# Optimization experiments

Measured on AMD Instinct MI355X. Metric: run time of the kernel, lower is better.

Reference implementation:

```python
import jax, jax.numpy as jnp
import numpy as np

D_MODEL, N_HEADS = 768, 12
D_K = D_MODEL // N_HEADS
NEG = -1e9


def setup_inputs() -> dict:
    key = jax.random.key(0)
    ks = jax.random.split(key, 12)
    B, S, D = 2, 4096, D_MODEL
    s = 1.0 / np.sqrt(D)
    inp = {
        'query': jax.random.normal(ks[0], (B, S, D), jnp.float32),
        'key': jax.random.normal(ks[1], (B, S, D), jnp.float32),
        'value': jax.random.normal(ks[2], (B, S, D), jnp.float32),
        'mask': jnp.ones((B, S), jnp.int32),
        'Wq': jax.random.normal(ks[3], (D, D), jnp.float32) * s,
        'bq': jnp.zeros((D,), jnp.float32),
        'Wk': jax.random.normal(ks[4], (D, D), jnp.float32) * s,
        'bk': jnp.zeros((D,), jnp.float32),
        'Wv': jax.random.normal(ks[5], (D, D), jnp.float32) * s,
        'bv': jnp.zeros((D,), jnp.float32),
        'Wo': jax.random.normal(ks[6], (D, D), jnp.float32) * s,
        'bo': jnp.zeros((D,), jnp.float32),
    }
    return inp


def reference(query, key, value, mask, Wq, bq, Wk, bk, Wv, bv, Wo, bo):
    B, Sq, D = query.shape
    Sk = key.shape[1]
    # torch Linear: x @ W.T + b; weights stored [out, in]
    def proj(x, W, b, S):
        return (x @ W.T + b).reshape(B, S, N_HEADS, D_K).transpose(0, 2, 1, 3)
    Q = proj(query, Wq, bq, Sq)   # [B,H,Sq,Dk]
    K = proj(key, Wk, bk, Sk)
    V = proj(value, Wv, bv, Sk)
    scores = jnp.einsum('bhqd,bhkd->bhqk', Q, K) / jnp.sqrt(jnp.float32(D_K))
    # padding mask on keys: [B,1,1,Sk]
    scores = jnp.where(mask[:, None, None, :] == 0, NEG, scores)
    # causal mask (triu, diagonal=1)
    causal = jnp.triu(jnp.ones((Sq, Sk), bool), k=1)
    scores = jnp.where(causal[None, None], NEG, scores)
    attn = jax.nn.softmax(scores, axis=-1)
    out = jnp.einsum('bhqk,bhkd->bhqd', attn, V)
    out = out.transpose(0, 2, 1, 3).reshape(B, Sq, D)
    return out @ Wo.T + bo
```

## Files before the change

### kernel.cpp

```cpp
#include <hip/hip_runtime.h>
#include <hip/hip_bf16.h>

#define D_MODEL 768
#define N_HEADS 12
#define D_K     64
#define NEG_INF (-1e9f)
#define SCALE_Q 0.1803368801111154f
#define W_ELEMS (D_MODEL * D_MODEL)

typedef __attribute__((ext_vector_type(8))) short          bf16x8;
typedef __attribute__((ext_vector_type(4))) float          floatx4;
typedef __attribute__((ext_vector_type(4))) unsigned short ushortx4;
typedef __attribute__((ext_vector_type(2))) unsigned int   uintx2;
typedef __attribute__((ext_vector_type(4))) unsigned int   uintx4;

static __device__ __forceinline__ unsigned short f2bf(float f) {
    unsigned u = __builtin_bit_cast(unsigned, f);
    u += 0x7FFFu + ((u >> 16) & 1u);
    return (unsigned short)(u >> 16);
}

static __device__ __forceinline__ float exp2_hw(float x) {
#if __has_builtin(__builtin_amdgcn_exp2f)
    return __builtin_amdgcn_exp2f(x);
#else
    return __builtin_exp2f(x);
#endif
}

static __device__ __forceinline__ float rcp_hw(float x) {
#if __has_builtin(__builtin_amdgcn_rcpf)
    return __builtin_amdgcn_rcpf(x);
#else
    return 1.f / x;
#endif
}

static __device__ __forceinline__ void gload_lds16(const void* g, void* l) {
    __builtin_amdgcn_global_load_lds(
        (const __attribute__((address_space(1))) void*)g,
        (__attribute__((address_space(3))) void*)l, 16, 0, 0);
}

__global__ __launch_bounds__(256) void convert_w4(
    const float* __restrict__ W0, const float* __restrict__ W1,
    const float* __restrict__ W2, const float* __restrict__ W3,
    unsigned short* __restrict__ out)
{
    const float* src[4] = {W0, W1, W2, W3};
    const float* W = src[blockIdx.y];
    unsigned short* o = out + (size_t)blockIdx.y * W_ELEMS;
    const int i = (blockIdx.x * 256 + threadIdx.x) * 4;
    float4 v = *(const float4*)(W + i);
    ushortx4 h = { f2bf(v.x), f2bf(v.y), f2bf(v.z), f2bf(v.w) };
    *(ushortx4*)(o + i) = h;
}

__global__ __launch_bounds__(256) void convert_a3(
    const float* __restrict__ A0, const float* __restrict__ A1,
    const float* __restrict__ A2,
    unsigned short* __restrict__ O0, unsigned short* __restrict__ O1,
    unsigned short* __restrict__ O2)
{
    const int z = blockIdx.y;
    const float* A = (z == 0) ? A0 : (z == 1) ? A1 : A2;
    unsigned short* O = (z == 0) ? O0 : (z == 1) ? O1 : O2;
    const int i = (blockIdx.x * 256 + threadIdx.x) * 4;
    float4 v = *(const float4*)(A + i);
    ushortx4 h = { f2bf(v.x), f2bf(v.y), f2bf(v.z), f2bf(v.w) };
    *(ushortx4*)(O + i) = h;
}

__global__ __launch_bounds__(256) void gemm128(
    const unsigned short* __restrict__ A0, const unsigned short* __restrict__ A1,
    const unsigned short* __restrict__ A2,
    const unsigned short* __restrict__ W0, const unsigned short* __restrict__ W1,
    const unsigned short* __restrict__ W2,
    const float* __restrict__ b0, const float* __restrict__ b1,
    const float* __restrict__ b2,
    void* __restrict__ C0, void* __restrict__ C1, void* __restrict__ C2,
    int S)
{
    __shared__ __align__(16) unsigned short As[128 * 32];
    __shared__ __align__(16) unsigned short Bs[128 * 32];

    const int z = blockIdx.z;
    const unsigned short* A = (z == 0) ? A0 : (z == 1) ? A1 : A2;
    const unsigned short* W = (z == 0) ? W0 : (z == 1) ? W1 : W2;
    const float* bias       = (z == 0) ? b0 : (z == 1) ? b1 : b2;
    void* C                 = (z == 0) ? C0 : (z == 1) ? C1 : C2;
    const float scale = (z == 0) ? SCALE_Q : 1.0f;
    const int mode = (z == 2) ? 3 : 1;

    const int tid  = threadIdx.x;
    const int wave = tid >> 6;
    const int lane = tid & 63;
    const int quad = lane >> 4;
    const int l16  = lane & 15;
    const int m0 = blockIdx.x * 128;
    const int n0 = blockIdx.y * 128;
    const int wm = (wave & 1) * 64;
    const int wn = (wave >> 1) * 64;
    const int sr = lane >> 2;
    const int sc = (lane & 3) << 3;

    const floatx4 zero4 = {0.f, 0.f, 0.f, 0.f};
    floatx4 acc[4][4];
    #pragma unroll
    for (int i = 0; i < 4; ++i)
        #pragma unroll
        for (int j = 0; j < 4; ++j) acc[i][j] = zero4;

    for (int k0 = 0; k0 < D_MODEL; k0 += 32) {
        #pragma unroll
        for (int c = 0; c < 2; ++c) {
            const int row = wave * 32 + c * 16;
            gload_lds16(A + (size_t)(m0 + row + sr) * D_MODEL + k0 + sc,
                        As + row * 32);
            gload_lds16(W + (size_t)(n0 + row + sr) * D_MODEL + k0 + sc,
                        Bs + row * 32);
        }
        __syncthreads();

        bf16x8 af[4], bfr[4];
        #pragma unroll
        for (int i = 0; i < 4; ++i)
            af[i] = *(const bf16x8*)(As + (wm + i * 16 + l16) * 32 + quad * 8);
        #pragma unroll
        for (int j = 0; j < 4; ++j)
            bfr[j] = *(const bf16x8*)(Bs + (wn + j * 16 + l16) * 32 + quad * 8);
        #pragma unroll
        for (int i = 0; i < 4; ++i)
            #pragma unroll
            for (int j = 0; j < 4; ++j)
                acc[i][j] = __builtin_amdgcn_mfma_f32_16x16x32_bf16(
                    bfr[j], af[i], acc[i][j], 0, 0, 0);
        __syncthreads();
    }

    #pragma unroll
    for (int i = 0; i < 4; ++i) {
        const int m = m0 + wm + i * 16 + l16;
        #pragma unroll
        for (int j = 0; j < 4; ++j) {
            const int nb = n0 + wn + j * 16 + quad * 4;
            const float4 bv = *(const float4*)(bias + nb);
            float v0 = (acc[i][j][0] + bv.x) * scale;
            float v1 = (acc[i][j][1] + bv.y) * scale;
            float v2 = (acc[i][j][2] + bv.z) * scale;
            float v3 = (acc[i][j][3] + bv.w) * scale;
            if (mode == 1) {
                ushortx4 o = {f2bf(v0), f2bf(v1), f2bf(v2), f2bf(v3)};
                *(ushortx4*)((unsigned short*)C + (size_t)m * D_MODEL + nb) = o;
            } else {
                const int bb = m / S, s = m - bb * S;
                const int hh = nb >> 6, d = nb & 63;
                unsigned short* base = (unsigned short*)C +
                    ((size_t)(bb * N_HEADS + hh) * D_K + d) * S + s;
                base[0]         = f2bf(v0);
                base[(size_t)S]     = f2bf(v1);
                base[(size_t)S * 2] = f2bf(v2);
                base[(size_t)S * 3] = f2bf(v3);
            }
        }
    }
}

__global__ __launch_bounds__(256) void gemm64o(
    const unsigned short* __restrict__ A,
    const unsigned short* __restrict__ W,
    const float* __restrict__ bias,
    float* __restrict__ C)
{
    __shared__ __align__(16) unsigned short As[64 * 32];
    __shared__ __align__(16) unsigned short Bs[128 * 32];

    const int tid  = threadIdx.x;
    const int wave = tid >> 6;
    const int lane = tid & 63;
    const int quad = lane >> 4;
    const int l16  = lane & 15;
    const int m0 = blockIdx.x * 64;
    const int n0 = blockIdx.y * 128;
    const int wn = wave * 32;
    const int sr = lane >> 2;
    const int sc = (lane & 3) << 3;

    const floatx4 zero4 = {0.f, 0.f, 0.f, 0.f};
    floatx4 acc[4][2];
    #pragma unroll
    for (int i = 0; i < 4; ++i)
        #pragma unroll
        for (int j = 0; j < 2; ++j) acc[i][j] = zero4;

    for (int k0 = 0; k0 < D_MODEL; k0 += 32) {
        if (wave < 2) {
            const int g0 = wave * 32;
            gload_lds16(A + (size_t)(m0 + g0 + sr) * D_MODEL + k0 + sc,
                        As + g0 * 32);
            gload_lds16(A + (size_t)(m0 + g0 + 16 + sr) * D_MODEL + k0 + sc,
                        As + (g0 + 16) * 32);
            const int bg = 96 + wave * 16;
            gload_lds16(W + (size_t)(n0 + bg + sr) * D_MODEL + k0 + sc,
                        Bs + bg * 32);
        } else {
            const int bg = (wave - 2) * 48;
            #pragma unroll
            for (int c = 0; c < 3; ++c)
                gload_lds16(W + (size_t)(n0 + bg + c * 16 + sr) * D_MODEL + k0 + sc,
                            Bs + (bg + c * 16) * 32);
        }
        __syncthreads();

        bf16x8 af[4], bfr[2];
        #pragma unroll
        for (int i = 0; i < 4; ++i)
            af[i] = *(const bf16x8*)(As + (i * 16 + l16) * 32 + quad * 8);
        #pragma unroll
        for (int j = 0; j < 2; ++j)
            bfr[j] = *(const bf16x8*)(Bs + (wn + j * 16 + l16) * 32 + quad * 8);
        #pragma unroll
        for (int i = 0; i < 4; ++i)
            #pragma unroll
            for (int j = 0; j < 2; ++j)
                acc[i][j] = __builtin_amdgcn_mfma_f32_16x16x32_bf16(
                    bfr[j], af[i], acc[i][j], 0, 0, 0);
        __syncthreads();
    }

    #pragma unroll
    for (int i = 0; i < 4; ++i) {
        const int m = m0 + i * 16 + l16;
        #pragma unroll
        for (int j = 0; j < 2; ++j) {
            const int nb = n0 + wn + j * 16 + quad * 4;
            const float4 bv = *(const float4*)(bias + nb);
            float4 o = {acc[i][j][0] + bv.x, acc[i][j][1] + bv.y,
                        acc[i][j][2] + bv.z, acc[i][j][3] + bv.w};
            *(float4*)(C + (size_t)m * D_MODEL + nb) = o;
        }
    }
}

__global__ __launch_bounds__(256) void flash_attn(
    const unsigned short* __restrict__ Qp,
    const unsigned short* __restrict__ Kp,
    const unsigned short* __restrict__ VpT,
    const int* __restrict__ mask,
    unsigned short* __restrict__ O,
    int S)
{
    __shared__ __align__(16) unsigned short Ks [128 * 64];
    __shared__ __align__(16) unsigned short Vts[64 * 128];
    __shared__ __align__(16) float mskf[128];

    const int L  = blockIdx.x;
    const int bh = L % 24;
    const int p  = L / 24;
    const int h  = bh % 12;
    const int b  = bh / 12;
    const int nqt = S >> 6;
    const int tid  = threadIdx.x;
    const int wave = tid >> 6;
    const int lane = tid & 63;
    const int quad = lane >> 4;
    const int l16  = lane & 15;
    const int sx   = (l16 & 7) << 3;
    const int qh   = wave & 1;
    const int kh2  = wave >> 1;

    const unsigned short* Kbase = Kp  + (size_t)(b * S) * D_MODEL + h * D_K;
    const unsigned short* Vbase = VpT + (size_t)(b * N_HEADS + h) * D_K * S;
    const int* mbase = mask + b * S;

    const int kgrow = wave * 32 + (lane >> 3);
    const int kgcol = ((lane & 7) ^ (lane >> 3)) << 3;
    const int vgrow = wave * 16 + (lane >> 4);
    const int vgc_e = ((lane & 15) ^ (lane >> 4)) << 3;
    const int vgc_o = ((lane & 15) ^ (4 + (lane >> 4))) << 3;

    const floatx4 zero4 = {0.f, 0.f, 0.f, 0.f};
    const short one_bf = (short)0x3F80;
    const bf16x8 ones = {one_bf, one_bf, one_bf, one_bf,
                         one_bf, one_bf, one_bf, one_bf};

    #pragma unroll
    for (int sel = 0; sel < 2; ++sel) {
        const int qt = sel ? (nqt - 1 - p) : p;
        const int q0 = qt * 64;

        bf16x8 qf[2][2];
        #pragma unroll
        for (int qg = 0; qg < 2; ++qg) {
            const size_t rowQ =
                (size_t)(b * S + q0 + qh * 32 + qg * 16 + l16) * D_MODEL + h * D_K;
            qf[qg][0] = *(const bf16x8*)(Qp + rowQ + quad * 8);
            qf[qg][1] = *(const bf16x8*)(Qp + rowQ + 32 + quad * 8);
        }

        floatx4 acc2[2][4];
        floatx4 accl[2];
        #pragma unroll
        for (int qg = 0; qg < 2; ++qg) {
            accl[qg] = zero4;
            #pragma unroll
            for (int dt = 0; dt < 4; ++dt) acc2[qg][dt] = zero4;
        }

        const int ni = (qt >> 1) + 1;
        for (int kt = 0; kt < ni; ++kt) {
            const int k0 = kt * 128;
            #pragma unroll
            for (int c = 0; c < 4; ++c) {
                gload_lds16(
                    Kbase + (size_t)(k0 + kgrow + c * 8) * D_MODEL + kgcol,
                    (char*)Ks + (wave * 4 + c) * 1024);
                const int vg = (c & 1) ? vgc_o : vgc_e;
                gload_lds16(
                    Vbase + (size_t)(vgrow + c * 4) * S + k0 + vg,
                    (char*)Vts + (wave * 4 + c) * 1024);
            }
            if (tid < 128)
                mskf[tid] = (mbase[k0 + tid] == 0) ? NEG_INF : 0.f;
            __syncthreads();

            floatx4 s[4][2];
            #pragma unroll
            for (int nt = 0; nt < 4; ++nt) {
                const int krow = kh2 * 64 + nt * 16 + l16;
                const unsigned short* kro = Ks + krow * 64;
                const bf16x8 kf0 = *(const bf16x8*)(kro + ((quad * 8) ^ sx));
                const bf16x8 kf1 = *(const bf16x8*)(kro + ((32 + quad * 8) ^ sx));
                const floatx4 cm =
                    *(const floatx4*)(mskf + kh2 * 64 + nt * 16 + quad * 4);
                #pragma unroll
                for (int qg = 0; qg < 2; ++qg) {
                    floatx4 c = cm;
                    c = __builtin_amdgcn_mfma_f32_16x16x32_bf16(kf0, qf[qg][0], c, 0, 0, 0);
                    c = __builtin_amdgcn_mfma_f32_16x16x32_bf16(kf1, qf[qg][1], c, 0, 0, 0);
                    s[nt][qg] = c;
                }
            }

            if (kt == ni - 1) {
                #pragma unroll
                for (int nt = 0; nt < 4; ++nt) {
                    const int kb = k0 + kh2 * 64 + nt * 16 + quad * 4;
                    #pragma unroll
                    for (int qg = 0; qg < 2; ++qg) {
                        const int qa = q0 + qh * 32 + qg * 16 + l16;
                        #pragma unroll
                        for (int r = 0; r < 4; ++r)
                            if (kb + r > qa) s[nt][qg][r] = NEG_INF;
                    }
                }
            }

            unsigned pk0[4][2], pk1[4][2];
            #pragma unroll
            for (int nt = 0; nt < 4; ++nt)
                #pragma unroll
                for (int qg = 0; qg < 2; ++qg) {
                    const float e0 = exp2_hw(s[nt][qg][0]);
                    const float e1 = exp2_hw(s[nt][qg][1]);
                    const float e2 = exp2_hw(s[nt][qg][2]);
                    const float e3 = exp2_hw(s[nt][qg][3]);
                    pk0[nt][qg] = __builtin_amdgcn_perm(
                        __builtin_bit_cast(unsigned, e1),
                        __builtin_bit_cast(unsigned, e0), 0x07060302u);
                    pk1[nt][qg] = __builtin_amdgcn_perm(
                        __builtin_bit_cast(unsigned, e3),
                        __builtin_bit_cast(unsigned, e2), 0x07060302u);
                }

            #pragma unroll
            for (int kh = 0; kh < 2; ++kh) {
                bf16x8 pf[2];
                #pragma unroll
                for (int qg = 0; qg < 2; ++qg) {
                    uintx2 a32 = __builtin_amdgcn_permlane32_swap(
                        pk0[2 * kh][qg], pk0[2 * kh + 1][qg], false, false);
                    uintx2 b32 = __builtin_amdgcn_permlane32_swap(
                        pk1[2 * kh][qg], pk1[2 * kh + 1][qg], false, false);
                    uintx2 a16 = __builtin_amdgcn_permlane16_swap(
                        a32[0], a32[1], false, false);
                    uintx2 b16 = __builtin_amdgcn_permlane16_swap(
                        b32[0], b32[1], false, false);
                    const uintx4 pw = {a16[0], b16[0], a16[1], b16[1]};
                    pf[qg] = __builtin_bit_cast(bf16x8, pw);
                }
                #pragma unroll
                for (int dt = 0; dt < 4; ++dt) {
                    const int vcol = kh2 * 64 + ((kh * 32 + quad * 8) ^ sx);
                    const bf16x8 vf =
                        *(const bf16x8*)(Vts + (dt * 16 + l16) * 128 + vcol);
                    #pragma unroll
                    for (int qg = 0; qg < 2; ++qg)
                        acc2[qg][dt] = __builtin_amdgcn_mfma_f32_16x16x32_bf16(
                            pf[qg], vf, acc2[qg][dt], 0, 0, 0);
                }
                #pragma unroll
                for (int qg = 0; qg < 2; ++qg)
                    accl[qg] = __builtin_amdgcn_mfma_f32_16x16x32_bf16(
                        pf[qg], ones, accl[qg], 0, 0, 0);
            }
            __syncthreads();
        }

        float* Kf = (float*)Ks;
        float* Vf = (float*)Vts;
        if (kh2 == 1) {
            #pragma unroll
            for (int qg = 0; qg < 2; ++qg) {
                #pragma unroll
                for (int dt = 0; dt < 4; ++dt)
                    *(floatx4*)(Kf + (qh * 8 + qg * 4 + dt) * 256 + lane * 4) =
                        acc2[qg][dt];
                *(floatx4*)(Vf + (qh * 2 + qg) * 256 + lane * 4) = accl[qg];
            }
        }
        __syncthreads();
        if (kh2 == 0) {
            #pragma unroll
            for (int qg = 0; qg < 2; ++qg) {
                accl[qg] += *(const floatx4*)(Vf + (qh * 2 + qg) * 256 + lane * 4);
                #pragma unroll
                for (int dt = 0; dt < 4; ++dt)
                    acc2[qg][dt] +=
                        *(const floatx4*)(Kf + (qh * 8 + qg * 4 + dt) * 256 + lane * 4);
                #pragma unroll
                for (int r = 0; r < 4; ++r) {
                    const float inv = rcp_hw(accl[qg][r]);
                    const int gq = q0 + qh * 32 + qg * 16 + quad * 4 + r;
                    const size_t base = (size_t)(b * S + gq) * D_MODEL + h * D_K;
                    #pragma unroll
                    for (int dt = 0; dt < 4; ++dt)
                        O[base + dt * 16 + l16] = f2bf(acc2[qg][dt][r] * inv);
                }
            }
        }
        __syncthreads();
    }
}

extern "C" void kernel_launch(void* const* d_in, const int* in_sizes, int n_in,
                              void* d_out, int out_size, void* d_ws, size_t ws_size,
                              hipStream_t stream) {
    const float* query = (const float*)d_in[0];
    const float* key   = (const float*)d_in[1];
    const float* value = (const float*)d_in[2];
    const int*   mask  = (const int*)d_in[3];
    const float* Wq = (const float*)d_in[4];
    const float* bq = (const float*)d_in[5];
    const float* Wk = (const float*)d_in[6];
    const float* bk = (const float*)d_in[7];
    const float* Wv = (const float*)d_in[8];
    const float* bv = (const float*)d_in[9];
    const float* Wo = (const float*)d_in[10];
    const float* bo = (const float*)d_in[11];

    const int B  = 2;
    const int BS = in_sizes[3];
    const int S  = BS / B;
    const int M  = BS;

    unsigned short* Qp  = (unsigned short*)d_ws;
    unsigned short* Kp  = Qp  + (size_t)M * D_MODEL;
    unsigned short* VpT = Kp  + (size_t)M * D_MODEL;
    unsigned short* Obf = VpT + (size_t)M * D_MODEL;
    unsigned short* Wbf = Obf + (size_t)M * D_MODEL;
    unsigned short* Wqb = Wbf;
    unsigned short* Wkb = Wbf + (size_t)W_ELEMS;
    unsigned short* Wvb = Wbf + (size_t)W_ELEMS * 2;
    unsigned short* Wob = Wbf + (size_t)W_ELEMS * 3;
    unsigned short* ka = (unsigned short*)d_out;
    unsigned short* va = ka + (size_t)M * D_MODEL;

    dim3 blk(256);
    convert_w4<<<dim3(W_ELEMS / 1024, 4), blk, 0, stream>>>(Wq, Wk, Wv, Wo, Wbf);
    convert_a3<<<dim3((M * D_MODEL) / 1024, 3), blk, 0, stream>>>(
        query, key, value, Obf, ka, va);

    gemm128<<<dim3(M / 128, D_MODEL / 128, 3), blk, 0, stream>>>(
        Obf, ka, va, Wqb, Wkb, Wvb, bq, bk, bv, Qp, Kp, VpT, S);

    flash_attn<<<768, blk, 0, stream>>>(Qp, Kp, VpT, mask, Obf, S);

    gemm64o<<<dim3(M / 64, D_MODEL / 128), blk, 0, stream>>>(
        Obf, Wob, bo, (float*)d_out);
}
```

Measured before the change: 295.0 us.

## Double-buffer 64-key K/V tiles in LDS and prefetch next tile during compute

The flash attention inner loop now uses 64-key tiles held in two LDS buffers. The next tile's K, V and mask are loaded while the current tile is computed, which removes the per-iteration load-then-sync stall, and one barrier per iteration replaces two. MFMA sections are wrapped in s_setprio to favour matrix work. The cost is twice as many iterations with less work each, plus somewhat finer causal-tail granularity.

```diff
diff --git a/kernel.cpp b/kernel.cpp
--- a/kernel.cpp
+++ b/kernel.cpp
@@ -250,9 +250,9 @@
     unsigned short* __restrict__ O,
     int S)
 {
-    __shared__ __align__(16) unsigned short Ks [128 * 64];
-    __shared__ __align__(16) unsigned short Vts[64 * 128];
-    __shared__ __align__(16) float mskf[128];
+    __shared__ __align__(16) unsigned short Ks [2][64 * 64];
+    __shared__ __align__(16) unsigned short Vts[2][64 * 64];
+    __shared__ __align__(16) float mskf[2][64];
 
     const int L  = blockIdx.x;
     const int bh = L % 24;
@@ -273,11 +273,8 @@
     const unsigned short* Vbase = VpT + (size_t)(b * N_HEADS + h) * D_K * S;
     const int* mbase = mask + b * S;
 
-    const int kgrow = wave * 32 + (lane >> 3);
-    const int kgcol = ((lane & 7) ^ (lane >> 3)) << 3;
-    const int vgrow = wave * 16 + (lane >> 4);
-    const int vgc_e = ((lane & 15) ^ (lane >> 4)) << 3;
-    const int vgc_o = ((lane & 15) ^ (4 + (lane >> 4))) << 3;
+    const int srow = wave * 8 + (lane >> 3);
+    const int sgc  = ((lane & 7) ^ (lane >> 3)) << 3;
 
     const floatx4 zero4 = {0.f, 0.f, 0.f, 0.f};
     const short one_bf = (short)0x3F80;
@@ -307,32 +304,47 @@
             for (int dt = 0; dt < 4; ++dt) acc2[qg][dt] = zero4;
         }
 
-        const int ni = (qt >> 1) + 1;
+        const int ni = qt + 1;
+
+        #pragma unroll
+        for (int c = 0; c < 2; ++c) {
+            gload_lds16(Kbase + (size_t)(c * 32 + srow) * D_MODEL + sgc,
+                        (char*)Ks[0] + (c * 4 + wave) * 1024);
+            gload_lds16(Vbase + (size_t)(c * 32 + srow) * S + sgc,
+                        (char*)Vts[0] + (c * 4 + wave) * 1024);
+        }
+        if (tid < 64) mskf[0][tid] = (mbase[tid] == 0) ? NEG_INF : 0.f;
+        __syncthreads();
+
         for (int kt = 0; kt < ni; ++kt) {
-            const int k0 = kt * 128;
-            #pragma unroll
-            for (int c = 0; c < 4; ++c) {
-                gload_lds16(
-                    Kbase + (size_t)(k0 + kgrow + c * 8) * D_MODEL + kgcol,
-                    (char*)Ks + (wave * 4 + c) * 1024);
-                const int vg = (c & 1) ? vgc_o : vgc_e;
-                gload_lds16(
-                    Vbase + (size_t)(vgrow + c * 4) * S + k0 + vg,
-                    (char*)Vts + (wave * 4 + c) * 1024);
-            }
-            if (tid < 128)
-                mskf[tid] = (mbase[k0 + tid] == 0) ? NEG_INF : 0.f;
-            __syncthreads();
-
-            floatx4 s[4][2];
-            #pragma unroll
-            for (int nt = 0; nt < 4; ++nt) {
-                const int krow = kh2 * 64 + nt * 16 + l16;
-                const unsigned short* kro = Ks + krow * 64;
+            const int k0 = kt * 64;
+            const int cur = kt & 1;
+
+            if (kt + 1 < ni) {
+                const int kn = k0 + 64;
+                #pragma unroll
+                for (int c = 0; c < 2; ++c) {
+                    gload_lds16(
+                        Kbase + (size_t)(kn + c * 32 + srow) * D_MODEL + sgc,
+                        (char*)Ks[cur ^ 1] + (c * 4 + wave) * 1024);
+                    gload_lds16(
+                        Vbase + (size_t)(c * 32 + srow) * S + kn + sgc,
+                        (char*)Vts[cur ^ 1] + (c * 4 + wave) * 1024);
+                }
+                if (tid < 64)
+                    mskf[cur ^ 1][tid] = (mbase[kn + tid] == 0) ? NEG_INF : 0.f;
+            }
+
+            floatx4 s[2][2];
+            __builtin_amdgcn_s_setprio(1);
+            #pragma unroll
+            for (int nt = 0; nt < 2; ++nt) {
+                const int krow = kh2 * 32 + nt * 16 + l16;
+                const unsigned short* kro = Ks[cur] + krow * 64;
                 const bf16x8 kf0 = *(const bf16x8*)(kro + ((quad * 8) ^ sx));
                 const bf16x8 kf1 = *(const bf16x8*)(kro + ((32 + quad * 8) ^ sx));
                 const floatx4 cm =
-                    *(const floatx4*)(mskf + kh2 * 64 + nt * 16 + quad * 4);
+                    *(const floatx4*)(&mskf[cur][kh2 * 32 + nt * 16 + quad * 4]);
                 #pragma unroll
                 for (int qg = 0; qg < 2; ++qg) {
                     floatx4 c = cm;
@@ -341,11 +353,12 @@
                     s[nt][qg] = c;
                 }
             }
+            __builtin_amdgcn_s_setprio(0);
 
             if (kt == ni - 1) {
                 #pragma unroll
-                for (int nt = 0; nt < 4; ++nt) {
-                    const int kb = k0 + kh2 * 64 + nt * 16 + quad * 4;
+                for (int nt = 0; nt < 2; ++nt) {
+                    const int kb = k0 + kh2 * 32 + nt * 16 + quad * 4;
                     #pragma unroll
                     for (int qg = 0; qg < 2; ++qg) {
                         const int qa = q0 + qh * 32 + qg * 16 + l16;
@@ -356,9 +369,9 @@
                 }
             }
 
-            unsigned pk0[4][2], pk1[4][2];
-            #pragma unroll
-            for (int nt = 0; nt < 4; ++nt)
+            unsigned pk0[2][2], pk1[2][2];
+            #pragma unroll
+            for (int nt = 0; nt < 2; ++nt)
                 #pragma unroll
                 for (int qg = 0; qg < 2; ++qg) {
                     const float e0 = exp2_hw(s[nt][qg][0]);
@@ -373,37 +386,37 @@
                         __builtin_bit_cast(unsigned, e2), 0x07060302u);
                 }
 
-            #pragma unroll
-            for (int kh = 0; kh < 2; ++kh) {
-                bf16x8 pf[2];
-                #pragma unroll
-                for (int qg = 0; qg < 2; ++qg) {
-                    uintx2 a32 = __builtin_amdgcn_permlane32_swap(
-                        pk0[2 * kh][qg], pk0[2 * kh + 1][qg], false, false);
-                    uintx2 b32 = __builtin_amdgcn_permlane32_swap(
-                        pk1[2 * kh][qg], pk1[2 * kh + 1][qg], false, false);
-                    uintx2 a16 = __builtin_amdgcn_permlane16_swap(
-                        a32[0], a32[1], false, false);
-                    uintx2 b16 = __builtin_amdgcn_permlane16_swap(
-                        b32[0], b32[1], false, false);
-                    const uintx4 pw = {a16[0], b16[0], a16[1], b16[1]};
-                    pf[qg] = __builtin_bit_cast(bf16x8, pw);
-                }
-                #pragma unroll
-                for (int dt = 0; dt < 4; ++dt) {
-                    const int vcol = kh2 * 64 + ((kh * 32 + quad * 8) ^ sx);
-                    const bf16x8 vf =
-                        *(const bf16x8*)(Vts + (dt * 16 + l16) * 128 + vcol);
-                    #pragma unroll
-                    for (int qg = 0; qg < 2; ++qg)
-                        acc2[qg][dt] = __builtin_amdgcn_mfma_f32_16x16x32_bf16(
-                            pf[qg], vf, acc2[qg][dt], 0, 0, 0);
-                }
+            bf16x8 pf[2];
+            #pragma unroll
+            for (int qg = 0; qg < 2; ++qg) {
+                uintx2 a32 = __builtin_amdgcn_permlane32_swap(
+                    pk0[0][qg], pk0[1][qg], false, false);
+                uintx2 b32 = __builtin_amdgcn_permlane32_swap(
+                    pk1[0][qg], pk1[1][qg], false, false);
+                uintx2 a16 = __builtin_amdgcn_permlane16_swap(
+                    a32[0], a32[1], false, false);
+                uintx2 b16 = __builtin_amdgcn_permlane16_swap(
+                    b32[0], b32[1], false, false);
+                const uintx4 pw = {a16[0], b16[0], a16[1], b16[1]};
+                pf[qg] = __builtin_bit_cast(bf16x8, pw);
+            }
+            __builtin_amdgcn_s_setprio(1);
+            #pragma unroll
+            for (int dt = 0; dt < 4; ++dt) {
+                const int vcol = (kh2 * 32 + quad * 8) ^ sx;
+                const bf16x8 vf =
+                    *(const bf16x8*)(Vts[cur] + (dt * 16 + l16) * 64 + vcol);
                 #pragma unroll
                 for (int qg = 0; qg < 2; ++qg)
-                    accl[qg] = __builtin_amdgcn_mfma_f32_16x16x32_bf16(
-                        pf[qg], ones, accl[qg], 0, 0, 0);
-            }
+                    acc2[qg][dt] = __builtin_amdgcn_mfma_f32_16x16x32_bf16(
+                        pf[qg], vf, acc2[qg][dt], 0, 0, 0);
+            }
+            #pragma unroll
+            for (int qg = 0; qg < 2; ++qg)
+                accl[qg] = __builtin_amdgcn_mfma_f32_16x16x32_bf16(
+                    pf[qg], ones, accl[qg], 0, 0, 0);
+            __builtin_amdgcn_s_setprio(0);
+
             __syncthreads();
         }
 
```

Result: faster. 286.8 us (-2.8%).
